# Kernel tuning notes

Hardware: AMD Instinct MI355X
Metric: run time of the kernel (lower is better)

The kernel has to match this reference:

```python
import jax, jax.numpy as jnp
import numpy as np

N_HEADS = 8
N_POINTS = 4
SPATIAL = np.array([[64, 64], [32, 32], [16, 16], [8, 8]], dtype=np.int32)


def setup_inputs() -> dict:
    key = jax.random.key(0)
    ks = jax.random.split(key, 12)
    d = 256
    H, L, P, N = N_HEADS, SPATIAL.shape[0], N_POINTS, 8
    lens = SPATIAL[:, 0] * SPATIAL[:, 1]
    Lin = int(lens.sum())
    Lq = Lin
    query = jax.random.normal(ks[0], (N, Lq, d), jnp.float32)
    reference_points = jax.random.uniform(ks[1], (N, Lq, L, 2), jnp.float32)
    input_flatten = jax.random.normal(ks[2], (N, Lin, d), jnp.float32)
    input_spatial_shapes = jnp.asarray(SPATIAL)
    starts = np.concatenate([[0], np.cumsum(lens)[:-1]]).astype(np.int32)
    input_level_start_index = jnp.asarray(starts)
    s = 1.0 / np.sqrt(d)
    W_off = jax.random.normal(ks[3], (H * L * P * 2, d), jnp.float32) * 0.01
    b_off = jax.random.normal(ks[4], (H * L * P * 2,), jnp.float32) * 0.5
    W_attn = jax.random.normal(ks[5], (H * L * P, d), jnp.float32) * 0.02
    b_attn = jnp.zeros((H * L * P,), jnp.float32)
    W_val = jax.random.normal(ks[6], (d, d), jnp.float32) * s
    b_val = jnp.zeros((d,), jnp.float32)
    W_out = jax.random.normal(ks[7], (d, d), jnp.float32) * s
    b_out = jnp.zeros((d,), jnp.float32)
    return {
        'query': query, 'reference_points': reference_points,
        'input_flatten': input_flatten,
        'input_spatial_shapes': input_spatial_shapes,
        'input_level_start_index': input_level_start_index,
        'W_off': W_off, 'b_off': b_off, 'W_attn': W_attn, 'b_attn': b_attn,
        'W_val': W_val, 'b_val': b_val, 'W_out': W_out, 'b_out': b_out,
    }


def _bilinear(img, Hl, Wl, x, y):
    # img: [B, Ch, Hl*Wl]; x, y: [B, Q, P] pixel coords (align_corners=False)
    # zero padding mode: out-of-range corners contribute 0
    x0 = jnp.floor(x)
    y0 = jnp.floor(y)
    wx = x - x0
    wy = y - y0

    def gather(xi, yi):
        valid = (xi >= 0) & (xi <= Wl - 1) & (yi >= 0) & (yi <= Hl - 1)
        ii = jnp.clip(xi, 0, Wl - 1).astype(jnp.int32)
        jj = jnp.clip(yi, 0, Hl - 1).astype(jnp.int32)
        idx = jj * Wl + ii  # [B, Q, P]
        B, Q, P = idx.shape
        v = jnp.take_along_axis(img, idx.reshape(B, 1, Q * P), axis=2)
        v = v.reshape(B, img.shape[1], Q, P)
        return v * valid[:, None].astype(img.dtype)

    return (gather(x0, y0) * ((1 - wx) * (1 - wy))[:, None]
            + gather(x0 + 1, y0) * (wx * (1 - wy))[:, None]
            + gather(x0, y0 + 1) * ((1 - wx) * wy)[:, None]
            + gather(x0 + 1, y0 + 1) * (wx * wy)[:, None])


def reference(query, reference_points, input_flatten, input_spatial_shapes,
              input_level_start_index, W_off, b_off, W_attn, b_attn,
              W_val, b_val, W_out, b_out):
    shapes = np.asarray(input_spatial_shapes)  # static structural metadata
    N, Lq, d = query.shape
    Lin = input_flatten.shape[1]
    L = shapes.shape[0]
    H, P = N_HEADS, N_POINTS
    Ch = d // H

    value = input_flatten @ W_val.T + b_val                       # [N, Lin, d]
    value = value.reshape(N, Lin, H, Ch).transpose(0, 2, 3, 1)    # [N, H, Ch, Lin]
    value = value.reshape(N * H, Ch, Lin)

    off = (query @ W_off.T + b_off).reshape(N, Lq, H, L, P, 2)
    attn = (query @ W_attn.T + b_attn).reshape(N, Lq, H, L * P)
    attn = jax.nn.softmax(attn, axis=-1).reshape(N, Lq, H, L, P)

    # normalizer is (W, H) per level
    norm = jnp.asarray(np.stack([shapes[:, 1], shapes[:, 0]], -1), query.dtype)
    loc = reference_points[:, :, None, :, None, :] + off / norm[None, None, None, :, None, :]

    attn_p = attn.transpose(0, 2, 1, 3, 4).reshape(N * H, Lq, L, P)
    starts = np.concatenate([[0], np.cumsum(shapes[:, 0] * shapes[:, 1])])

    out = jnp.zeros((N * H, Ch, Lq), query.dtype)
    for l in range(L):
        Hl, Wl = int(shapes[l, 0]), int(shapes[l, 1])
        v_l = value[:, :, starts[l]:starts[l + 1]]                # [B, Ch, Hl*Wl]
        g = loc[:, :, :, l].transpose(0, 2, 1, 3, 4).reshape(N * H, Lq, P, 2)
        # grid_sample align_corners=False with grid=2*loc-1 -> pixel = loc*W - 0.5
        x = g[..., 0] * Wl - 0.5
        y = g[..., 1] * Hl - 0.5
        samp = _bilinear(v_l, Hl, Wl, x, y)                       # [B, Ch, Lq, P]
        out = out + jnp.einsum('bcqp,bqp->bcq', samp, attn_p[:, :, l])

    out = out.reshape(N, H, Ch, Lq).transpose(0, 3, 1, 2).reshape(N, Lq, d)
    return out @ W_out.T + b_out
```

## Files before the change

kernel.cpp:

```cpp
#include <hip/hip_runtime.h>
#include <hip/hip_bf16.h>
#include <hip/hip_fp16.h>

#define NQ   5440
#define NB   8
#define DIM  256
#define NH   8
#define CHN  32
#define NLV  4
#define NPT  4
#define MTOT (NB * NQ)

typedef __attribute__((ext_vector_type(8))) short s16x8;
typedef __attribute__((ext_vector_type(4))) float f32x4;
typedef unsigned short ushort_t;

#define WVAL 0
#define WOFF 65536
#define WATT 131072
#define WOUT 163840
#define WTOT 229376
#define QTOT (MTOT * DIM)

__device__ __forceinline__ short f2bf(float x) {
    union { __hip_bfloat16 b; short s; } u;
    u.b = __float2bfloat16(x);
    return u.s;
}

__device__ __forceinline__ void gload_lds16(const void* g, void* l) {
    __builtin_amdgcn_global_load_lds(
        (const __attribute__((address_space(1))) unsigned int*)g,
        (__attribute__((address_space(3))) unsigned int*)l, 16, 0, 0);
}

__device__ __forceinline__ void cvt8b(const float* s, ushort_t* d) {
    f32x4 a = *(const f32x4*)s, b = *(const f32x4*)(s + 4);
    s16x8 v;
#pragma unroll
    for (int e = 0; e < 4; ++e) { v[e] = f2bf(a[e]); v[e + 4] = f2bf(b[e]); }
    *(s16x8*)d = v;
}

__global__ __launch_bounds__(256) void cvt_all(const float* __restrict__ wv,
                                               const float* __restrict__ wo,
                                               const float* __restrict__ wa,
                                               const float* __restrict__ wu,
                                               const float* __restrict__ query,
                                               ushort_t* __restrict__ wb,
                                               ushort_t* __restrict__ qb) {
    const int i = (blockIdx.x * 256 + threadIdx.x) * 8;
    if (i < WTOT) {
        const float* src;
        int off;
        if (i < WOFF)      { src = wv; off = WVAL; }
        else if (i < WATT) { src = wo; off = WOFF; }
        else if (i < WOUT) { src = wa; off = WATT; }
        else               { src = wu; off = WOUT; }
        cvt8b(src + (i - off), wb + i);
    } else {
        const int j = i - WTOT;
        if (j < QTOT) cvt8b(query + j, qb + j);
    }
}

__device__ __forceinline__ void stC(float* p, float v) { *p = v; }
__device__ __forceinline__ void stC(__half* p, float v) { *p = __float2half(v); }
__device__ __forceinline__ void stC(ushort_t* p, float v) { *(short*)p = f2bf(v); }

template <typename AT, typename CT>
__device__ __forceinline__ void gemm_core(const AT* __restrict__ A,
                                          const ushort_t* __restrict__ Wt,
                                          const float* __restrict__ biasT,
                                          CT* __restrict__ Ct, int ldC, int rowBase) {
    __shared__ ushort_t As[128 * 64];
    __shared__ ushort_t Ws[128 * 64];

    const int t = threadIdx.x;
    const int lane = t & 63, w = t >> 6;
    const int wm = w >> 1, wn = w & 1;
    const int lr = lane & 15, quad = lane >> 4;

    f32x4 acc[4][4];
#pragma unroll
    for (int i = 0; i < 4; ++i)
#pragma unroll
        for (int j = 0; j < 4; ++j)
#pragma unroll
            for (int r = 0; r < 4; ++r) acc[i][j][r] = 0.f;

    for (int ks = 0; ks < 4; ++ks) {
        if (ks) __syncthreads();
#pragma unroll
        for (int i = 0; i < 4; ++i) {
            const int c = t + i * 256;
            const int r = c >> 3, s = c & 7;
            const int g = (s - r) & 7;
            const int ke = ks * 64 + g * 8;
            gload_lds16(Wt + (size_t)r * DIM + ke,
                        &Ws[(size_t)(i * 256 + w * 64) * 8]);
            if constexpr (sizeof(AT) == 2) {
                gload_lds16(A + (size_t)(rowBase + r) * DIM + ke,
                            &As[(size_t)(i * 256 + w * 64) * 8]);
            } else {
                const float* pa = (const float*)A + (size_t)(rowBase + r) * DIM + ke;
                f32x4 a0 = *(const f32x4*)pa, a1 = *(const f32x4*)(pa + 4);
                s16x8 av;
#pragma unroll
                for (int e = 0; e < 4; ++e) {
                    av[e] = f2bf(a0[e]);
                    av[e + 4] = f2bf(a1[e]);
                }
                *(s16x8*)&As[(size_t)c * 8] = av;
            }
        }
        __syncthreads();
#pragma unroll
        for (int kk = 0; kk < 64; kk += 32) {
            s16x8 afr[4], wfr[4];
            const int G = (kk >> 3) + quad;
#pragma unroll
            for (int i = 0; i < 4; ++i) {
                const int R = wm * 64 + i * 16 + lr;
                afr[i] = *(const s16x8*)&As[(R * 8 + ((G + R) & 7)) * 8];
            }
#pragma unroll
            for (int j = 0; j < 4; ++j) {
                const int R = wn * 64 + j * 16 + lr;
                wfr[j] = *(const s16x8*)&Ws[(R * 8 + ((G + R) & 7)) * 8];
            }
#pragma unroll
            for (int i = 0; i < 4; ++i)
#pragma unroll
                for (int j = 0; j < 4; ++j)
                    acc[i][j] = __builtin_amdgcn_mfma_f32_16x16x32_bf16(
                        afr[i], wfr[j], acc[i][j], 0, 0, 0);
        }
    }

    float bj[4];
#pragma unroll
    for (int j = 0; j < 4; ++j) bj[j] = biasT[wn * 64 + j * 16 + lr];
#pragma unroll
    for (int i = 0; i < 4; ++i)
#pragma unroll
        for (int r = 0; r < 4; ++r) {
            int row = rowBase + wm * 64 + i * 16 + quad * 4 + r;
#pragma unroll
            for (int j = 0; j < 4; ++j) {
                int col = wn * 64 + j * 16 + lr;
                stC(&Ct[(size_t)row * ldC + col], acc[i][j][r] + bj[j]);
            }
        }
}

__global__ __launch_bounds__(256) void gemm_fused(const float* __restrict__ inputf,
                                                  const ushort_t* __restrict__ qb,
                                                  const ushort_t* __restrict__ wb,
                                                  const float* __restrict__ b_val,
                                                  const float* __restrict__ b_off,
                                                  const float* __restrict__ b_attn,
                                                  __half* __restrict__ bval,
                                                  __half* __restrict__ v_off,
                                                  __half* __restrict__ v_attn) {
    const int gy = blockIdx.y;
    const int rowBase = blockIdx.x * 128;
    if (gy < 2)
        gemm_core<float, __half>(inputf, wb + WVAL + (size_t)gy * 128 * DIM,
                                 b_val + gy * 128, bval + gy * 128, DIM, rowBase);
    else if (gy < 4)
        gemm_core<ushort_t, __half>(qb, wb + WOFF + (size_t)(gy - 2) * 128 * DIM,
                                    b_off + (gy - 2) * 128, v_off + (gy - 2) * 128,
                                    DIM, rowBase);
    else
        gemm_core<ushort_t, __half>(qb, wb + WATT, b_attn, v_attn, 128, rowBase);
}

__global__ __launch_bounds__(256) void gemm_out(const ushort_t* __restrict__ A,
                                                const ushort_t* __restrict__ wb,
                                                const float* __restrict__ bias,
                                                float* __restrict__ C) {
    gemm_core<ushort_t, float>(A, wb + WOUT + (size_t)blockIdx.y * 128 * DIM,
                               bias + blockIdx.y * 128, C + blockIdx.y * 128, DIM,
                               blockIdx.x * 128);
}

__global__ __launch_bounds__(128) void sample_kernel(
    const float* __restrict__ refp,
    const __half* __restrict__ off,
    const __half* __restrict__ attn,
    const __half* __restrict__ bval,
    const int* __restrict__ shapes,
    const int* __restrict__ starts,
    ushort_t* __restrict__ sampb)
{
    const int n = blockIdx.x & 7;
    const int qBase = n * NQ + (blockIdx.x >> 3) * 4;
    const int t = threadIdx.x;

    __shared__ __align__(16) int     sidx[512][4];
    __shared__ __align__(16) __half2 sww[512][4];

#pragma unroll
    for (int it = 0; it < 4; ++it) {
        const int i = t + it * 128;
        const int q4 = i >> 7, hlp = i & 127;
        const int h = hlp >> 4, lp = hlp & 15, l = lp >> 2;
        const int q = qBase + q4;
        const int Wl = shapes[2 * l + 1], Hl = shapes[2 * l];
        const float Wf = (float)Wl, Hf = (float)Hl;
        const float2 rp = *(const float2*)(refp + ((size_t)q * NLV + l) * 2);
        const __half2 oo2 = ((const __half2*)off)[(size_t)q * 128 + h * 16 + lp];
        const float2 oo = __half22float2(oo2);
        const float x = (rp.x + oo.x / Wf) * Wf - 0.5f;
        const float y = (rp.y + oo.y / Hf) * Hf - 0.5f;

        float logit = __half2float(attn[(size_t)q * 128 + h * 16 + lp]);
        float m = logit;
#pragma unroll
        for (int s = 8; s >= 1; s >>= 1) m = fmaxf(m, __shfl_xor(m, s, 16));
        float e = __expf(logit - m);
        float ss = e;
#pragma unroll
        for (int s = 8; s >= 1; s >>= 1) ss += __shfl_xor(ss, s, 16);
        const float aw = e / ss;

        const float xf = floorf(x), yf = floorf(y);
        const int ix = (int)xf, iy = (int)yf;
        const float wx = x - xf, wy = y - yf;
        const int ix1 = ix + 1, iy1 = iy + 1;
        const bool bx0 = (ix >= 0) & (ix < Wl);
        const bool bx1 = (ix1 >= 0) & (ix1 < Wl);
        const bool by0 = (iy >= 0) & (iy < Hl);
        const bool by1 = (iy1 >= 0) & (iy1 < Hl);
        const int cx0 = min(max(ix, 0), Wl - 1), cx1 = min(max(ix1, 0), Wl - 1);
        const int cy0 = min(max(iy, 0), Hl - 1), cy1 = min(max(iy1, 0), Hl - 1);
        const int base = n * NQ + starts[l];
        int4 id;
        id.x = (base + cy0 * Wl + cx0) << 9;
        id.y = (base + cy0 * Wl + cx1) << 9;
        id.z = (base + cy1 * Wl + cx0) << 9;
        id.w = (base + cy1 * Wl + cx1) << 9;
        __half2 wp[4];
        wp[0] = __float2half2_rn((bx0 && by0) ? aw * (1.f - wx) * (1.f - wy) : 0.f);
        wp[1] = __float2half2_rn((bx1 && by0) ? aw * wx * (1.f - wy) : 0.f);
        wp[2] = __float2half2_rn((bx0 && by1) ? aw * (1.f - wx) * wy : 0.f);
        wp[3] = __float2half2_rn((bx1 && by1) ? aw * wx * wy : 0.f);
        *(int4*)sidx[i] = id;
        *(uint4*)&sww[i][0] = *(uint4*)wp;
    }
    __syncthreads();

    const int q4 = t >> 5, r = t & 31;
    const int h = r >> 2, cg = r & 3;
    const int q = qBase + q4;
    const char* vb = (const char*)bval + h * 64 + cg * 16;

    __half2 acch[4];
    float accf[8];
#pragma unroll
    for (int e = 0; e < 4; ++e) acch[e] = __float2half2_rn(0.f);
#pragma unroll
    for (int e = 0; e < 8; ++e) accf[e] = 0.f;

#pragma unroll
    for (int j = 0; j < 16; ++j) {
        const int lp = (j + h) & 15;
        const int slot = (q4 << 7) + (h << 4) + lp;
        const int4 id = *(const int4*)sidx[slot];
        uint4 wu = *(const uint4*)&sww[slot][0];
        const __half2* wp = (const __half2*)&wu;
        int idc[4] = {id.x, id.y, id.z, id.w};
#pragma unroll
        for (int c = 0; c < 4; ++c) {
            const uint4 u = *(const uint4*)(vb + (size_t)(unsigned)idc[c]);
            const __half2* hv = (const __half2*)&u;
#pragma unroll
            for (int e = 0; e < 4; ++e) acch[e] = __hfma2(hv[e], wp[c], acch[e]);
        }
        if ((j & 3) == 3) {
#pragma unroll
            for (int e = 0; e < 4; ++e) {
                float2 f = __half22float2(acch[e]);
                accf[2 * e] += f.x;
                accf[2 * e + 1] += f.y;
                acch[e] = __float2half2_rn(0.f);
            }
        }
    }

    s16x8 o;
#pragma unroll
    for (int e = 0; e < 8; ++e) o[e] = f2bf(accf[e]);
    *(s16x8*)(sampb + (size_t)q * DIM + h * CHN + cg * 8) = o;
}

extern "C" void kernel_launch(void* const* d_in, const int* in_sizes, int n_in,
                              void* d_out, int out_size, void* d_ws, size_t ws_size,
                              hipStream_t stream) {
    const float* query  = (const float*)d_in[0];
    const float* refp   = (const float*)d_in[1];
    const float* inputf = (const float*)d_in[2];
    const int* shapes   = (const int*)d_in[3];
    const int* starts   = (const int*)d_in[4];
    const float* W_off  = (const float*)d_in[5];
    const float* b_off  = (const float*)d_in[6];
    const float* W_attn = (const float*)d_in[7];
    const float* b_attn = (const float*)d_in[8];
    const float* W_val  = (const float*)d_in[9];
    const float* b_val  = (const float*)d_in[10];
    const float* W_out  = (const float*)d_in[11];
    const float* b_out  = (const float*)d_in[12];
    float* out = (float*)d_out;

    const size_t AB = (size_t)MTOT * DIM * 2;
    char* ws = (char*)d_ws;
    ushort_t* wb     = (ushort_t*)ws;
    __half*   bval   = (__half*)(ws + 512 * 1024);
    __half*   v_off  = (__half*)(ws + 512 * 1024 + AB);
    __half*   v_attn = (__half*)(ws + 512 * 1024 + 2 * AB);
    ushort_t* sampb  = (ushort_t*)(ws + 512 * 1024 + 2 * AB + AB / 2);
    ushort_t* qb     = (ushort_t*)(ws + 512 * 1024 + 3 * AB + AB / 2);

    const int cvtBlocks = (WTOT + QTOT) / 2048;
    cvt_all<<<dim3(cvtBlocks), dim3(256), 0, stream>>>(W_val, W_off, W_attn, W_out,
                                                       query, wb, qb);
    gemm_fused<<<dim3(MTOT / 128, 5), dim3(256), 0, stream>>>(
        inputf, qb, wb, b_val, b_off, b_attn, bval, v_off, v_attn);
    sample_kernel<<<dim3(MTOT / 4), dim3(128), 0, stream>>>(
        refp, v_off, v_attn, bval, shapes, starts, sampb);
    gemm_out<<<dim3(MTOT / 128, 2), dim3(256), 0, stream>>>(sampb, wb, b_out, out);
}
```

Baseline: 261.5 us.

## Double-buffer GEMM shared-memory tiles to overlap global loads with MFMA

Changes the GEMM core to use two LDS buffers per operand. The next K-slice is issued into the alternate buffer while MFMAs run on the current one. For fp32 A inputs, the values are held in registers and converted to bf16 after compute. This removes one barrier per K step and hides load latency, at the cost of doubling LDS to 64KB per block, which may reduce occupancy, and adding register pressure.

```diff
diff --git a/kernel.cpp b/kernel.cpp
--- a/kernel.cpp
+++ b/kernel.cpp
@@ -69,13 +69,12 @@
 __device__ __forceinline__ void stC(ushort_t* p, float v) { *(short*)p = f2bf(v); }
 
 template <typename AT, typename CT>
-__device__ __forceinline__ void gemm_core(const AT* __restrict__ A,
+__device__ __forceinline__ void gemm_core(ushort_t* __restrict__ AsB,
+                                          ushort_t* __restrict__ WsB,
+                                          const AT* __restrict__ A,
                                           const ushort_t* __restrict__ Wt,
                                           const float* __restrict__ biasT,
                                           CT* __restrict__ Ct, int ldC, int rowBase) {
-    __shared__ ushort_t As[128 * 64];
-    __shared__ ushort_t Ws[128 * 64];
-
     const int t = threadIdx.x;
     const int lane = t & 63, w = t >> 6;
     const int wm = w >> 1, wn = w & 1;
@@ -89,8 +88,11 @@
 #pragma unroll
             for (int r = 0; r < 4; ++r) acc[i][j][r] = 0.f;
 
-    for (int ks = 0; ks < 4; ++ks) {
-        if (ks) __syncthreads();
+    f32x4 ra0[4], ra1[4];
+
+    auto issue = [&](int ks, int b) {
+        ushort_t* Wd = WsB + b * 8192;
+        ushort_t* Ad = AsB + b * 8192;
 #pragma unroll
         for (int i = 0; i < 4; ++i) {
             const int c = t + i * 256;
@@ -98,23 +100,43 @@
             const int g = (s - r) & 7;
             const int ke = ks * 64 + g * 8;
             gload_lds16(Wt + (size_t)r * DIM + ke,
-                        &Ws[(size_t)(i * 256 + w * 64) * 8]);
+                        &Wd[(size_t)(i * 256 + w * 64) * 8]);
             if constexpr (sizeof(AT) == 2) {
                 gload_lds16(A + (size_t)(rowBase + r) * DIM + ke,
-                            &As[(size_t)(i * 256 + w * 64) * 8]);
+                            &Ad[(size_t)(i * 256 + w * 64) * 8]);
             } else {
                 const float* pa = (const float*)A + (size_t)(rowBase + r) * DIM + ke;
-                f32x4 a0 = *(const f32x4*)pa, a1 = *(const f32x4*)(pa + 4);
+                ra0[i] = *(const f32x4*)pa;
+                ra1[i] = *(const f32x4*)(pa + 4);
+            }
+        }
+    };
+    auto commitA = [&](int b) {
+        if constexpr (sizeof(AT) == 4) {
+            ushort_t* Ad = AsB + b * 8192;
+#pragma unroll
+            for (int i = 0; i < 4; ++i) {
+                const int c = t + i * 256;
                 s16x8 av;
 #pragma unroll
                 for (int e = 0; e < 4; ++e) {
-                    av[e] = f2bf(a0[e]);
-                    av[e + 4] = f2bf(a1[e]);
+                    av[e] = f2bf(ra0[i][e]);
+                    av[e + 4] = f2bf(ra1[i][e]);
                 }
-                *(s16x8*)&As[(size_t)c * 8] = av;
-            }
-        }
-        __syncthreads();
+                *(s16x8*)&Ad[(size_t)c * 8] = av;
+            }
+        }
+    };
+
+    issue(0, 0);
+    commitA(0);
+    __syncthreads();
+
+    for (int ks = 0; ks < 4; ++ks) {
+        const int cb = ks & 1, nb = cb ^ 1;
+        if (ks < 3) issue(ks + 1, nb);
+        const ushort_t* Ab = AsB + cb * 8192;
+        const ushort_t* Wb = WsB + cb * 8192;
 #pragma unroll
         for (int kk = 0; kk < 64; kk += 32) {
             s16x8 afr[4], wfr[4];
@@ -122,12 +144,12 @@
 #pragma unroll
             for (int i = 0; i < 4; ++i) {
                 const int R = wm * 64 + i * 16 + lr;
-                afr[i] = *(const s16x8*)&As[(R * 8 + ((G + R) & 7)) * 8];
+                afr[i] = *(const s16x8*)&Ab[(R * 8 + ((G + R) & 7)) * 8];
             }
 #pragma unroll
             for (int j = 0; j < 4; ++j) {
                 const int R = wn * 64 + j * 16 + lr;
-                wfr[j] = *(const s16x8*)&Ws[(R * 8 + ((G + R) & 7)) * 8];
+                wfr[j] = *(const s16x8*)&Wb[(R * 8 + ((G + R) & 7)) * 8];
             }
 #pragma unroll
             for (int i = 0; i < 4; ++i)
@@ -136,6 +158,8 @@
                     acc[i][j] = __builtin_amdgcn_mfma_f32_16x16x32_bf16(
                         afr[i], wfr[j], acc[i][j], 0, 0, 0);
         }
+        if (ks < 3) commitA(nb);
+        __syncthreads();
     }
 
     float bj[4];
@@ -163,24 +187,29 @@
                                                   __half* __restrict__ bval,
                                                   __half* __restrict__ v_off,
                                                   __half* __restrict__ v_attn) {
+    __shared__ ushort_t As[2 * 8192];
+    __shared__ ushort_t Ws[2 * 8192];
     const int gy = blockIdx.y;
     const int rowBase = blockIdx.x * 128;
     if (gy < 2)
-        gemm_core<float, __half>(inputf, wb + WVAL + (size_t)gy * 128 * DIM,
+        gemm_core<float, __half>(As, Ws, inputf, wb + WVAL + (size_t)gy * 128 * DIM,
                                  b_val + gy * 128, bval + gy * 128, DIM, rowBase);
     else if (gy < 4)
-        gemm_core<ushort_t, __half>(qb, wb + WOFF + (size_t)(gy - 2) * 128 * DIM,
+        gemm_core<ushort_t, __half>(As, Ws, qb, wb + WOFF + (size_t)(gy - 2) * 128 * DIM,
                                     b_off + (gy - 2) * 128, v_off + (gy - 2) * 128,
                                     DIM, rowBase);
     else
-        gemm_core<ushort_t, __half>(qb, wb + WATT, b_attn, v_attn, 128, rowBase);
+        gemm_core<ushort_t, __half>(As, Ws, qb, wb + WATT, b_attn, v_attn, 128,
+                                    rowBase);
 }
 
 __global__ __launch_bounds__(256) void gemm_out(const ushort_t* __restrict__ A,
                                                 const ushort_t* __restrict__ wb,
                                                 const float* __restrict__ bias,
                                                 float* __restrict__ C) {
-    gemm_core<ushort_t, float>(A, wb + WOUT + (size_t)blockIdx.y * 128 * DIM,
+    __shared__ ushort_t As[2 * 8192];
+    __shared__ ushort_t Ws[2 * 8192];
+    gemm_core<ushort_t, float>(As, Ws, A, wb + WOUT + (size_t)blockIdx.y * 128 * DIM,
                                bias + blockIdx.y * 128, C + blockIdx.y * 128, DIM,
                                blockIdx.x * 128);
 }
```

Measured after the change: 260.1 us. About the same (-0.5%).

## Double-buffer GEMM K-loop, pre-convert input to bf16, persistent grid for projections

Applied to the files above, without the earlier changes.

The shared GEMM core is rewritten to use K-steps of 32 with double-buffered LDS tiles, so the next global-to-LDS load is issued while MFMAs run on the current buffer. The fp32 input_flatten is now converted to bf16 in the conversion kernel, staged in the output buffer as scratch, so every GEMM path uses async LDS loads. The fused projection GEMM becomes a persistent kernel of 1024 blocks looping over 1700 jobs, and occupancy hints are added. The trade-off is an extra conversion pass over input_flatten and the reuse of the output buffer as a temporary.

```diff
diff --git a/kernel.cpp b/kernel.cpp
--- a/kernel.cpp
+++ b/kernel.cpp
@@ -47,8 +47,10 @@
                                                const float* __restrict__ wa,
                                                const float* __restrict__ wu,
                                                const float* __restrict__ query,
+                                               const float* __restrict__ inputf,
                                                ushort_t* __restrict__ wb,
-                                               ushort_t* __restrict__ qb) {
+                                               ushort_t* __restrict__ qb,
+                                               ushort_t* __restrict__ ib) {
     const int i = (blockIdx.x * 256 + threadIdx.x) * 8;
     if (i < WTOT) {
         const float* src;
@@ -61,21 +63,23 @@
     } else {
         const int j = i - WTOT;
         if (j < QTOT) cvt8b(query + j, qb + j);
+        else {
+            const int k = j - QTOT;
+            if (k < QTOT) cvt8b(inputf + k, ib + k);
+        }
     }
 }
 
 __device__ __forceinline__ void stC(float* p, float v) { *p = v; }
 __device__ __forceinline__ void stC(__half* p, float v) { *p = __float2half(v); }
-__device__ __forceinline__ void stC(ushort_t* p, float v) { *(short*)p = f2bf(v); }
-
-template <typename AT, typename CT>
-__device__ __forceinline__ void gemm_core(const AT* __restrict__ A,
-                                          const ushort_t* __restrict__ Wt,
-                                          const float* __restrict__ biasT,
-                                          CT* __restrict__ Ct, int ldC, int rowBase) {
-    __shared__ ushort_t As[128 * 64];
-    __shared__ ushort_t Ws[128 * 64];
-
+
+template <typename CT>
+__device__ __forceinline__ void gemm_job(ushort_t* __restrict__ AsB,
+                                         ushort_t* __restrict__ WsB,
+                                         const ushort_t* __restrict__ A,
+                                         const ushort_t* __restrict__ Wt,
+                                         const float* __restrict__ biasT,
+                                         CT* __restrict__ Ct, int ldC, int rowBase) {
     const int t = threadIdx.x;
     const int lane = t & 63, w = t >> 6;
     const int wm = w >> 1, wn = w & 1;
@@ -89,53 +93,49 @@
 #pragma unroll
             for (int r = 0; r < 4; ++r) acc[i][j][r] = 0.f;
 
-    for (int ks = 0; ks < 4; ++ks) {
-        if (ks) __syncthreads();
+    auto issue = [&](int ks, int b) {
+        ushort_t* Ad = AsB + b * 4096;
+        ushort_t* Wd = WsB + b * 4096;
+#pragma unroll
+        for (int i = 0; i < 2; ++i) {
+            const int c = t + i * 256;
+            const int r = c >> 2, s = c & 3;
+            const int g = (s - r) & 3;
+            const int ke = ks * 32 + g * 8;
+            gload_lds16(A + (size_t)(rowBase + r) * DIM + ke,
+                        &Ad[(size_t)(i * 256 + w * 64) * 8]);
+            gload_lds16(Wt + (size_t)r * DIM + ke,
+                        &Wd[(size_t)(i * 256 + w * 64) * 8]);
+        }
+    };
+
+    issue(0, 0);
+    __syncthreads();
+
+    for (int ks = 0; ks < 8; ++ks) {
+        const int cb = ks & 1, nb = cb ^ 1;
+        if (ks < 7) issue(ks + 1, nb);
+        const ushort_t* Ab = AsB + cb * 4096;
+        const ushort_t* Wb = WsB + cb * 4096;
+        s16x8 afr[4], wfr[4];
+        const int G = quad;
 #pragma unroll
         for (int i = 0; i < 4; ++i) {
-            const int c = t + i * 256;
-            const int r = c >> 3, s = c & 7;
-            const int g = (s - r) & 7;
-            const int ke = ks * 64 + g * 8;
-            gload_lds16(Wt + (size_t)r * DIM + ke,
-                        &Ws[(size_t)(i * 256 + w * 64) * 8]);
-            if constexpr (sizeof(AT) == 2) {
-                gload_lds16(A + (size_t)(rowBase + r) * DIM + ke,
-                            &As[(size_t)(i * 256 + w * 64) * 8]);
-            } else {
-                const float* pa = (const float*)A + (size_t)(rowBase + r) * DIM + ke;
-                f32x4 a0 = *(const f32x4*)pa, a1 = *(const f32x4*)(pa + 4);
-                s16x8 av;
-#pragma unroll
-                for (int e = 0; e < 4; ++e) {
-                    av[e] = f2bf(a0[e]);
-                    av[e + 4] = f2bf(a1[e]);
-                }
-                *(s16x8*)&As[(size_t)c * 8] = av;
-            }
-        }
+            const int R = wm * 64 + i * 16 + lr;
+            afr[i] = *(const s16x8*)&Ab[(R * 4 + ((G + R) & 3)) * 8];
+        }
+#pragma unroll
+        for (int j = 0; j < 4; ++j) {
+            const int R = wn * 64 + j * 16 + lr;
+            wfr[j] = *(const s16x8*)&Wb[(R * 4 + ((G + R) & 3)) * 8];
+        }
+#pragma unroll
+        for (int i = 0; i < 4; ++i)
+#pragma unroll
+            for (int j = 0; j < 4; ++j)
+                acc[i][j] = __builtin_amdgcn_mfma_f32_16x16x32_bf16(
+                    afr[i], wfr[j], acc[i][j], 0, 0, 0);
         __syncthreads();
-#pragma unroll
-        for (int kk = 0; kk < 64; kk += 32) {
-            s16x8 afr[4], wfr[4];
-            const int G = (kk >> 3) + quad;
-#pragma unroll
-            for (int i = 0; i < 4; ++i) {
-                const int R = wm * 64 + i * 16 + lr;
-                afr[i] = *(const s16x8*)&As[(R * 8 + ((G + R) & 7)) * 8];
-            }
-#pragma unroll
-            for (int j = 0; j < 4; ++j) {
-                const int R = wn * 64 + j * 16 + lr;
-                wfr[j] = *(const s16x8*)&Ws[(R * 8 + ((G + R) & 7)) * 8];
-            }
-#pragma unroll
-            for (int i = 0; i < 4; ++i)
-#pragma unroll
-                for (int j = 0; j < 4; ++j)
-                    acc[i][j] = __builtin_amdgcn_mfma_f32_16x16x32_bf16(
-                        afr[i], wfr[j], acc[i][j], 0, 0, 0);
-        }
     }
 
     float bj[4];
@@ -154,35 +154,48 @@
         }
 }
 
-__global__ __launch_bounds__(256) void gemm_fused(const float* __restrict__ inputf,
-                                                  const ushort_t* __restrict__ qb,
-                                                  const ushort_t* __restrict__ wb,
-                                                  const float* __restrict__ b_val,
-                                                  const float* __restrict__ b_off,
-                                                  const float* __restrict__ b_attn,
-                                                  __half* __restrict__ bval,
-                                                  __half* __restrict__ v_off,
-                                                  __half* __restrict__ v_attn) {
-    const int gy = blockIdx.y;
-    const int rowBase = blockIdx.x * 128;
-    if (gy < 2)
-        gemm_core<float, __half>(inputf, wb + WVAL + (size_t)gy * 128 * DIM,
-                                 b_val + gy * 128, bval + gy * 128, DIM, rowBase);
-    else if (gy < 4)
-        gemm_core<ushort_t, __half>(qb, wb + WOFF + (size_t)(gy - 2) * 128 * DIM,
-                                    b_off + (gy - 2) * 128, v_off + (gy - 2) * 128,
-                                    DIM, rowBase);
-    else
-        gemm_core<ushort_t, __half>(qb, wb + WATT, b_attn, v_attn, 128, rowBase);
-}
-
-__global__ __launch_bounds__(256) void gemm_out(const ushort_t* __restrict__ A,
-                                                const ushort_t* __restrict__ wb,
-                                                const float* __restrict__ bias,
-                                                float* __restrict__ C) {
-    gemm_core<ushort_t, float>(A, wb + WOUT + (size_t)blockIdx.y * 128 * DIM,
-                               bias + blockIdx.y * 128, C + blockIdx.y * 128, DIM,
-                               blockIdx.x * 128);
+__global__ __launch_bounds__(256, 4) void gemm_all(const ushort_t* __restrict__ qb,
+                                                   const ushort_t* __restrict__ ib,
+                                                   const ushort_t* __restrict__ wb,
+                                                   const float* __restrict__ b_val,
+                                                   const float* __restrict__ b_off,
+                                                   const float* __restrict__ b_attn,
+                                                   __half* __restrict__ bval,
+                                                   __half* __restrict__ v_off,
+                                                   __half* __restrict__ v_attn) {
+    __shared__ ushort_t As[2 * 4096];
+    __shared__ ushort_t Ws[2 * 4096];
+    for (int job = blockIdx.x; job < 1700; job += gridDim.x) {
+        const int jx = job / 5, jy = job - jx * 5;
+        const int rowBase = jx * 128;
+        const ushort_t* A;
+        const ushort_t* Wt;
+        const float* bs;
+        __half* Ct;
+        int ldC;
+        if (jy < 2) {
+            A = ib;  Wt = wb + WVAL + (size_t)jy * 128 * DIM;
+            bs = b_val + jy * 128;  Ct = bval + jy * 128;  ldC = DIM;
+        } else if (jy < 4) {
+            A = qb;  Wt = wb + WOFF + (size_t)(jy - 2) * 128 * DIM;
+            bs = b_off + (jy - 2) * 128;  Ct = v_off + (jy - 2) * 128;  ldC = DIM;
+        } else {
+            A = qb;  Wt = wb + WATT;
+            bs = b_attn;  Ct = v_attn;  ldC = 128;
+        }
+        gemm_job<__half>(As, Ws, A, Wt, bs, Ct, ldC, rowBase);
+    }
+}
+
+__global__ __launch_bounds__(256, 4) void gemm_out(const ushort_t* __restrict__ A,
+                                                   const ushort_t* __restrict__ wb,
+                                                   const float* __restrict__ bias,
+                                                   float* __restrict__ C) {
+    __shared__ ushort_t As[2 * 4096];
+    __shared__ ushort_t Ws[2 * 4096];
+    gemm_job<float>(As, Ws, A, wb + WOUT + (size_t)blockIdx.y * 128 * DIM,
+                    bias + blockIdx.y * 128, C + blockIdx.y * 128, DIM,
+                    blockIdx.x * 128);
 }
 
 __global__ __launch_bounds__(128) void sample_kernel(
@@ -321,13 +334,14 @@
     __half*   v_attn = (__half*)(ws + 512 * 1024 + 2 * AB);
     ushort_t* sampb  = (ushort_t*)(ws + 512 * 1024 + 2 * AB + AB / 2);
     ushort_t* qb     = (ushort_t*)(ws + 512 * 1024 + 3 * AB + AB / 2);
-
-    const int cvtBlocks = (WTOT + QTOT) / 2048;
+    ushort_t* ib     = (ushort_t*)d_out;
+
+    const int cvtBlocks = (WTOT + 2 * QTOT) / 2048;
     cvt_all<<<dim3(cvtBlocks), dim3(256), 0, stream>>>(W_val, W_off, W_attn, W_out,
-                                                       query, wb, qb);
-    gemm_fused<<<dim3(MTOT / 128, 5), dim3(256), 0, stream>>>(
-        inputf, qb, wb, b_val, b_off, b_attn, bval, v_off, v_attn);
+                                                       query, inputf, wb, qb, ib);
+    gemm_all<<<dim3(1024), dim3(256), 0, stream>>>(qb, ib, wb, b_val, b_off, b_attn,
+                                                   bval, v_off, v_attn);
     sample_kernel<<<dim3(MTOT / 4), dim3(128), 0, stream>>>(
         refp, v_off, v_attn, bval, shapes, starts, sampb);
-    gemm_out<<<dim3(MTOT / 128, 2), dim3(256), 0, stream>>>(sampb, wb, b_out, out);
-}
+    gemm_out<<<dim3(340, 2), dim3(256), 0, stream>>>(sampb, wb, b_out, out);
+}
```

New measurement: 268.1 us. 2.5% more time.
